# Performance work log

Measured on AMD Instinct MI355X. Metric: run time of the kernel, lower is better.

## Reference

```python
import jax, jax.numpy as jnp
import numpy as np
import math

ALPHA = 1.0  # surrogate-gradient sharpness, self.alpha() == 1.0

@jax.custom_vjp
def spike(x):
    # Heaviside forward (PiecewiseQuadratic.apply forward)
    return (x >= 0).astype(x.dtype)

def _spike_fwd(x):
    return spike(x), x

def _spike_bwd(x, g):
    # piecewise-quadratic surrogate: g'(x) = alpha - alpha^2*|x| for |x| < 1/alpha, else 0
    sg = jnp.where(jnp.abs(x) < 1.0 / ALPHA, -(ALPHA ** 2) * jnp.abs(x) + ALPHA, 0.0)
    return (g * sg.astype(x.dtype),)

spike.defvjp(_spike_fwd, _spike_bwd)


def setup_inputs() -> dict:
    key = jax.random.key(0)
    kx = jax.random.fold_in(key, 0)
    B, T, N = 64, 64, 8192
    x = jax.random.normal(kx, (B, T, N), dtype=jnp.float32)
    # parameters per __init__: tau=2.0 -> stored param log(1/(tau-1)) = 0.0
    tau_p = jnp.array([math.log(1.0 / (2.0 - 1.0))], dtype=jnp.float32)
    lamb = jnp.array([0.2], dtype=jnp.float32)
    th = jnp.array([1.0], dtype=jnp.float32)  # non-learnable
    return {"x": x, "tau_p": tau_p, "lamb": lamb, "th": th}


def reference(x, tau_p, lamb, th):
    sig = jax.nn.sigmoid(tau_p)  # scalar leak factor, shape [1]
    xt = jnp.swapaxes(x, 0, 1)   # [T, B, N] for scan over time

    def step(last, x_t):
        u = last * sig + x_t
        s = spike(u - th)
        new_last = (u + lamb * (u - last)) * (1.0 - s)  # momentum + hard reset
        return new_last, s

    last0 = jnp.zeros_like(x[:, 0])
    _, out = jax.lax.scan(step, last0, xt)  # out: [T, B, N]
    return jnp.swapaxes(out, 0, 1)         # [B, T, N]
```

## Files before the change

kernel.cpp:

```cpp
#include <hip/hip_runtime.h>


#define LIF_B 64
#define LIF_T 64
#define LIF_N 8192
#define NV (LIF_N / 4)

__global__ __launch_bounds__(256) void lif_fwd_kernel(
    const float4* __restrict__ x,
    const float*  __restrict__ tau_p,
    const float*  __restrict__ lamb_p,
    const float*  __restrict__ th_p,
    float4* __restrict__ out)
{
    const int tid = blockIdx.x * blockDim.x + threadIdx.x;
    const int b   = tid / NV;
    const int n4  = tid - b * NV;

    const float sig  = 1.0f / (1.0f + expf(-tau_p[0]));
    const float lamb = lamb_p[0];
    const float th   = th_p[0];

    float4 last = make_float4(0.f, 0.f, 0.f, 0.f);
    size_t base = (size_t)b * LIF_T * NV + n4;

#pragma unroll 8
    for (int t = 0; t < LIF_T; ++t) {
        const size_t idx = base + (size_t)t * NV;
        float4 xv = x[idx];
        float4 sv;

        {
            float u  = __fadd_rn(__fmul_rn(last.x, sig), xv.x);
            float s  = (u >= th) ? 1.0f : 0.0f;
            float nl = __fmul_rn(__fadd_rn(u, __fmul_rn(lamb, __fsub_rn(u, last.x))),
                                 __fsub_rn(1.0f, s));
            last.x = nl; sv.x = s;
        }
        {
            float u  = __fadd_rn(__fmul_rn(last.y, sig), xv.y);
            float s  = (u >= th) ? 1.0f : 0.0f;
            float nl = __fmul_rn(__fadd_rn(u, __fmul_rn(lamb, __fsub_rn(u, last.y))),
                                 __fsub_rn(1.0f, s));
            last.y = nl; sv.y = s;
        }
        {
            float u  = __fadd_rn(__fmul_rn(last.z, sig), xv.z);
            float s  = (u >= th) ? 1.0f : 0.0f;
            float nl = __fmul_rn(__fadd_rn(u, __fmul_rn(lamb, __fsub_rn(u, last.z))),
                                 __fsub_rn(1.0f, s));
            last.z = nl; sv.z = s;
        }
        {
            float u  = __fadd_rn(__fmul_rn(last.w, sig), xv.w);
            float s  = (u >= th) ? 1.0f : 0.0f;
            float nl = __fmul_rn(__fadd_rn(u, __fmul_rn(lamb, __fsub_rn(u, last.w))),
                                 __fsub_rn(1.0f, s));
            last.w = nl; sv.w = s;
        }

        out[idx] = sv;
    }
}

extern "C" void kernel_launch(void* const* d_in, const int* in_sizes, int n_in,
                              void* d_out, int out_size, void* d_ws, size_t ws_size,
                              hipStream_t stream) {
    (void)in_sizes; (void)n_in; (void)out_size; (void)d_ws; (void)ws_size;

    const float4* x     = (const float4*)d_in[0];
    const float*  tau_p = (const float*)d_in[1];
    const float*  lamb  = (const float*)d_in[2];
    const float*  th    = (const float*)d_in[3];
    float4*       out   = (float4*)d_out;

    const int total_threads = LIF_B * NV;
    const int block = 256;
    const int grid  = total_threads / block;

    lif_fwd_kernel<<<grid, block, 0, stream>>>(x, tau_p, lamb, th, out);
}
```

Measured before the change: 243.5 us.

## Use float2 per thread with batched 16-step loads and nontemporal stores

Each thread now handles two neurons instead of four, doubling the thread count to 131072. It loads 16 timesteps of input up front before running the serial recurrence, which gives more memory-level parallelism. Output stores are nontemporal so the write-only spike tensor does not pollute the cache. The risks are narrower 8-byte accesses, which may lower per-instruction efficiency, and higher register use for the 16-element buffer.

```diff
diff --git a/kernel.cpp b/kernel.cpp
--- a/kernel.cpp
+++ b/kernel.cpp
@@ -4,62 +4,54 @@
 #define LIF_B 64
 #define LIF_T 64
 #define LIF_N 8192
-#define NV (LIF_N / 4)
+#define NV2 (LIF_N / 2)
+#define UNROLL 16
+
+typedef float f2 __attribute__((ext_vector_type(2)));
 
 __global__ __launch_bounds__(256) void lif_fwd_kernel(
-    const float4* __restrict__ x,
-    const float*  __restrict__ tau_p,
-    const float*  __restrict__ lamb_p,
-    const float*  __restrict__ th_p,
-    float4* __restrict__ out)
+    const f2* __restrict__ x,
+    const float* __restrict__ tau_p,
+    const float* __restrict__ lamb_p,
+    const float* __restrict__ th_p,
+    f2* __restrict__ out)
 {
     const int tid = blockIdx.x * blockDim.x + threadIdx.x;
-    const int b   = tid / NV;
-    const int n4  = tid - b * NV;
+    const int b   = tid / NV2;
+    const int n2  = tid - b * NV2;
 
     const float sig  = 1.0f / (1.0f + expf(-tau_p[0]));
     const float lamb = lamb_p[0];
     const float th   = th_p[0];
 
-    float4 last = make_float4(0.f, 0.f, 0.f, 0.f);
-    size_t base = (size_t)b * LIF_T * NV + n4;
+    float lx = 0.0f, ly = 0.0f;
+    const size_t base = (size_t)b * LIF_T * NV2 + n2;
 
-#pragma unroll 8
-    for (int t = 0; t < LIF_T; ++t) {
-        const size_t idx = base + (size_t)t * NV;
-        float4 xv = x[idx];
-        float4 sv;
-
-        {
-            float u  = __fadd_rn(__fmul_rn(last.x, sig), xv.x);
-            float s  = (u >= th) ? 1.0f : 0.0f;
-            float nl = __fmul_rn(__fadd_rn(u, __fmul_rn(lamb, __fsub_rn(u, last.x))),
-                                 __fsub_rn(1.0f, s));
-            last.x = nl; sv.x = s;
+    for (int tb = 0; tb < LIF_T; tb += UNROLL) {
+        f2 xv[UNROLL];
+#pragma unroll
+        for (int i = 0; i < UNROLL; ++i) {
+            xv[i] = x[base + (size_t)(tb + i) * NV2];
         }
-        {
-            float u  = __fadd_rn(__fmul_rn(last.y, sig), xv.y);
-            float s  = (u >= th) ? 1.0f : 0.0f;
-            float nl = __fmul_rn(__fadd_rn(u, __fmul_rn(lamb, __fsub_rn(u, last.y))),
-                                 __fsub_rn(1.0f, s));
-            last.y = nl; sv.y = s;
+#pragma unroll
+        for (int i = 0; i < UNROLL; ++i) {
+            f2 sv;
+            {
+                float u  = __fadd_rn(__fmul_rn(lx, sig), xv[i].x);
+                float s  = (u >= th) ? 1.0f : 0.0f;
+                lx = __fmul_rn(__fadd_rn(u, __fmul_rn(lamb, __fsub_rn(u, lx))),
+                               __fsub_rn(1.0f, s));
+                sv.x = s;
+            }
+            {
+                float u  = __fadd_rn(__fmul_rn(ly, sig), xv[i].y);
+                float s  = (u >= th) ? 1.0f : 0.0f;
+                ly = __fmul_rn(__fadd_rn(u, __fmul_rn(lamb, __fsub_rn(u, ly))),
+                               __fsub_rn(1.0f, s));
+                sv.y = s;
+            }
+            __builtin_nontemporal_store(sv, &out[base + (size_t)(tb + i) * NV2]);
         }
-        {
-            float u  = __fadd_rn(__fmul_rn(last.z, sig), xv.z);
-            float s  = (u >= th) ? 1.0f : 0.0f;
-            float nl = __fmul_rn(__fadd_rn(u, __fmul_rn(lamb, __fsub_rn(u, last.z))),
-                                 __fsub_rn(1.0f, s));
-            last.z = nl; sv.z = s;
-        }
-        {
-            float u  = __fadd_rn(__fmul_rn(last.w, sig), xv.w);
-            float s  = (u >= th) ? 1.0f : 0.0f;
-            float nl = __fmul_rn(__fadd_rn(u, __fmul_rn(lamb, __fsub_rn(u, last.w))),
-                                 __fsub_rn(1.0f, s));
-            last.w = nl; sv.w = s;
-        }
-
-        out[idx] = sv;
     }
 }
 
@@ -68,13 +60,13 @@
                               hipStream_t stream) {
     (void)in_sizes; (void)n_in; (void)out_size; (void)d_ws; (void)ws_size;
 
-    const float4* x     = (const float4*)d_in[0];
-    const float*  tau_p = (const float*)d_in[1];
-    const float*  lamb  = (const float*)d_in[2];
-    const float*  th    = (const float*)d_in[3];
-    float4*       out   = (float4*)d_out;
+    const f2*    x     = (const f2*)d_in[0];
+    const float* tau_p = (const float*)d_in[1];
+    const float* lamb  = (const float*)d_in[2];
+    const float* th    = (const float*)d_in[3];
+    f2*          out   = (f2*)d_out;
 
-    const int total_threads = LIF_B * NV;
+    const int total_threads = LIF_B * NV2;
     const int block = 256;
     const int grid  = total_threads / block;
 
```

Result: faster. 234.8 us (-3.6%).
